# Kernel tuning notes

Hardware: AMD Instinct MI355X
Metric: run time of the kernel (lower is better)

## Reference

```python
import jax, jax.numpy as jnp
import numpy as np

N = 32767      # 2**15 - 1 nodes: complete binary tree, parent(i) = (i-1)//2
IN = 512       # in_channels
H = 256        # hidden_dim
OUT = 1        # output_dim
DEPTH = 15     # number of topological levels (static)


def setup_inputs() -> dict:
    key = jax.random.key(0)
    ks = jax.random.split(key, 8)
    x = jax.random.normal(ks[0], (N, IN), dtype=jnp.float32)
    # complete binary tree edge list: edge_index[0]=child, edge_index[1]=parent
    src = jnp.arange(1, N, dtype=jnp.int32)
    dst = (src - 1) // 2
    edge_index = jnp.stack([src, dst])  # [2, N-1]
    s = 1.0 / np.sqrt(H)  # torch LSTMCell/Linear default uniform init scale
    W_ih = jax.random.uniform(ks[1], (4 * H, IN), minval=-s, maxval=s, dtype=jnp.float32)
    W_hh = jax.random.uniform(ks[2], (4 * H, H), minval=-s, maxval=s, dtype=jnp.float32)
    b_ih = jax.random.uniform(ks[3], (4 * H,), minval=-s, maxval=s, dtype=jnp.float32)
    b_hh = jax.random.uniform(ks[4], (4 * H,), minval=-s, maxval=s, dtype=jnp.float32)
    W_fc = jax.random.uniform(ks[5], (OUT, H), minval=-s, maxval=s, dtype=jnp.float32)
    b_fc = jax.random.uniform(ks[6], (OUT,), minval=-s, maxval=s, dtype=jnp.float32)
    return {"x": x, "edge_index": edge_index, "W_ih": W_ih, "W_hh": W_hh,
            "b_ih": b_ih, "b_hh": b_hh, "W_fc": W_fc, "b_fc": b_fc}


def reference(x, edge_index, W_ih, W_hh, b_ih, b_hh, W_fc, b_fc):
    src, dst = edge_index[0], edge_index[1]
    # children count per parent (matches torch children_count loop)
    cnt = jax.ops.segment_sum(jnp.ones_like(src, dtype=x.dtype), dst, num_segments=N)
    cnt = jnp.maximum(cnt, 1.0)[:, None]  # [N,1]; leaves get zero child state anyway
    h = jnp.zeros((N, H), dtype=x.dtype)
    c = jnp.zeros((N, H), dtype=x.dtype)
    # topological sweep: deepest level first (children processed before parents)
    for d in range(DEPTH - 1, -1, -1):
        lo = 2 ** d - 1
        hi = min(2 ** (d + 1) - 1, N)  # level d node index range (static)
        # mean of already-computed child h/c states, gathered via edge list
        mean_h = jax.ops.segment_sum(h[src], dst, num_segments=N)[lo:hi] / cnt[lo:hi]
        mean_c = jax.ops.segment_sum(c[src], dst, num_segments=N)[lo:hi] / cnt[lo:hi]
        # torch LSTMCell: gates in (i, f, g, o) order
        gates = x[lo:hi] @ W_ih.T + b_ih + mean_h @ W_hh.T + b_hh  # [n_level, 4H]
        i, f, g, o = jnp.split(gates, 4, axis=-1)
        i, f, o = jax.nn.sigmoid(i), jax.nn.sigmoid(f), jax.nn.sigmoid(o)
        g = jnp.tanh(g)
        c_new = f * mean_c + i * g
        h_new = o * jnp.tanh(c_new)
        h = h.at[lo:hi].set(h_new)
        c = c.at[lo:hi].set(c_new)
    pooled = jnp.mean(h, axis=0, keepdims=True)  # [1, H]
    out = pooled @ W_fc.T + b_fc                 # [1, 1]
    return out.squeeze(-1)                       # [1]
```

## Files before the change

### kernel.cpp

```cpp
#include <hip/hip_runtime.h>
#include <hip/hip_cooperative_groups.h>
#include <math.h>

namespace cg = cooperative_groups;


#define N_NODES 32767
#define N_LEAF0 16383
#define IN_C    512
#define H_C     256

typedef __bf16 bf16x8 __attribute__((ext_vector_type(8)));
typedef __bf16 bf16x4 __attribute__((ext_vector_type(4)));
typedef float  f32x4  __attribute__((ext_vector_type(4)));

__device__ __forceinline__ void gload_lds16(const void* g, void* l) {
    __builtin_amdgcn_global_load_lds(
        (const __attribute__((address_space(1))) unsigned int*)g,
        (__attribute__((address_space(3))) unsigned int*)l,
        16, 0, 0);
}

__device__ __forceinline__ float fast_rcp(float x) { return __builtin_amdgcn_rcpf(x); }
__device__ __forceinline__ float sigm(float x)     { return fast_rcp(1.f + __expf(-x)); }
__device__ __forceinline__ float tanh_fast(float x){ return 2.f * fast_rcp(1.f + __expf(-2.f * x)) - 1.f; }

__global__ __launch_bounds__(256)
void conv2(const float* __restrict__ a, __bf16* __restrict__ da, int n8a,
           const float* __restrict__ b, __bf16* __restrict__ db, int n8b,
           float* __restrict__ hsum)
{
    if (blockIdx.x == 0 && threadIdx.x < 256) hsum[threadIdx.x] = 0.f;
    const int total = n8a + n8b;
    for (int i = blockIdx.x * 256 + threadIdx.x; i < total; i += gridDim.x * 256) {
        const float* s; __bf16* d; int j;
        if (i < n8a) { s = a; d = da; j = i; }
        else         { s = b; d = db; j = i - n8a; }
        const float4* s4 = (const float4*)s;
        const float4 v0 = s4[2 * j];
        const float4 v1 = s4[2 * j + 1];
        bf16x8 o;
        o[0] = (__bf16)v0.x; o[1] = (__bf16)v0.y; o[2] = (__bf16)v0.z; o[3] = (__bf16)v0.w;
        o[4] = (__bf16)v1.x; o[5] = (__bf16)v1.y; o[6] = (__bf16)v1.z; o[7] = (__bf16)v1.w;
        *(bf16x8*)(d + 8 * j) = o;
    }
}

__global__ __launch_bounds__(256)
void bulk_xw(const float* __restrict__ x,
             const __bf16* __restrict__ wih,
             const float* __restrict__ b_ih,
             const float* __restrict__ b_hh,
             __bf16* __restrict__ hb,
             float* __restrict__ c,
             __bf16* __restrict__ gx,
             float* __restrict__ hsum)
{
    __shared__ __bf16 As[128 * 64];
    __shared__ __bf16 Bs[128 * 64];
    __shared__ float  hs[32];

    const int t    = threadIdx.x;
    const int lane = t & 63;
    const int wv   = t >> 6;
    const int wm   = wv >> 1;
    const int wn   = wv & 1;
    const int quad = lane >> 4;
    const int l15  = lane & 15;

    if (t < 32) hs[t] = 0.f;

    const int i  = blockIdx.x;
    const int cb = (i >> 3) & 7;
    const int mt = (i & 7) | ((i >> 6) << 3);
    const int m0 = mt * 128;

    f32x4 acc[4][4];
#pragma unroll
    for (int mi = 0; mi < 4; ++mi)
#pragma unroll
        for (int ni = 0; ni < 4; ++ni) acc[mi][ni] = (f32x4)0.f;

    const int arow = t >> 1;
    const int kh   = (t & 1) * 32;
    const int anode = min(m0 + arow, N_NODES - 1);
    const float* xrow = x + (size_t)anode * IN_C + kh;
    float4 xr[8];
#pragma unroll
    for (int j = 0; j < 8; ++j) xr[j] = ((const float4*)xrow)[j];

    for (int k0 = 0; k0 < IN_C; k0 += 64) {
#pragma unroll
        for (int e = 0; e < 4; ++e) {
            const int ch = (wv * 4 + e) * 64 + lane;
            const int nl = ch >> 3;
            const int k8 = (ch & 7) ^ (nl & 7);
            const int q  = (nl >> 4) & 3;
            const int cc = (nl & 15) | ((nl >> 6) << 4);
            const int grow = q * H_C + cb * 32 + cc;
            gload_lds16(wih + (size_t)grow * IN_C + k0 + k8 * 8,
                        (char*)Bs + (wv * 4 + e) * 1024);
        }
#pragma unroll
        for (int j = 0; j < 4; ++j) {
            const float4 v0 = xr[2 * j], v1 = xr[2 * j + 1];
            bf16x8 o;
            o[0] = (__bf16)v0.x; o[1] = (__bf16)v0.y; o[2] = (__bf16)v0.z; o[3] = (__bf16)v0.w;
            o[4] = (__bf16)v1.x; o[5] = (__bf16)v1.y; o[6] = (__bf16)v1.z; o[7] = (__bf16)v1.w;
            const int cs = ((kh >> 3) + j) ^ (arow & 7);
            *(bf16x8*)(As + arow * 64 + cs * 8) = o;
        }
        __syncthreads();
        if (k0 + 64 < IN_C) {
            const float4* xs = (const float4*)(xrow + k0 + 64);
#pragma unroll
            for (int j = 0; j < 8; ++j) xr[j] = xs[j];
        }
#pragma unroll
        for (int ks = 0; ks < 2; ++ks) {
            bf16x8 af[4], bfr[4];
#pragma unroll
            for (int mi = 0; mi < 4; ++mi) {
                const int row = wm * 64 + mi * 16 + l15;
                af[mi] = *(const bf16x8*)(As + row * 64 + (((ks * 4 + quad) ^ (row & 7)) << 3));
            }
#pragma unroll
            for (int ni = 0; ni < 4; ++ni) {
                const int row = wn * 64 + ni * 16 + l15;
                bfr[ni] = *(const bf16x8*)(Bs + row * 64 + (((ks * 4 + quad) ^ (row & 7)) << 3));
            }
#pragma unroll
            for (int mi = 0; mi < 4; ++mi)
#pragma unroll
                for (int ni = 0; ni < 4; ++ni)
                    acc[mi][ni] = __builtin_amdgcn_mfma_f32_16x16x32_bf16(
                        af[mi], bfr[ni], acc[mi][ni], 0, 0, 0);
        }
        __syncthreads();
    }

    const int CH = cb * 32 + wn * 16 + l15;
    float bs4[4];
#pragma unroll
    for (int q = 0; q < 4; ++q) bs4[q] = b_ih[q * H_C + CH] + b_hh[q * H_C + CH];

    float lh = 0.f;
#pragma unroll
    for (int mi = 0; mi < 4; ++mi) {
#pragma unroll
        for (int r = 0; r < 4; ++r) {
            const int m = m0 + wm * 64 + mi * 16 + quad * 4 + r;
            if (m >= N_NODES) continue;
            if (m >= N_LEAF0) {
                const float gi = sigm(acc[mi][0][r] + bs4[0]);
                const float gg = tanh_fast(acc[mi][2][r] + bs4[2]);
                const float go = sigm(acc[mi][3][r] + bs4[3]);
                const float cn = gi * gg;
                const float hn = go * tanh_fast(cn);
                c[(size_t)m * H_C + CH] = cn;
                hb[(size_t)m * H_C + CH] = (__bf16)hn;
                lh += hn;
            } else {
                bf16x4 o;
#pragma unroll
                for (int q = 0; q < 4; ++q) o[q] = (__bf16)acc[mi][q][r];
                *(bf16x4*)(gx + ((size_t)m * H_C + CH) * 4) = o;
            }
        }
    }
    atomicAdd(&hs[wn * 16 + l15], lh);
    __syncthreads();
    if (t < 32) atomicAdd(&hsum[cb * 32 + t], hs[t]);
}

__device__ __forceinline__ void level_tile(
    const __bf16* __restrict__ whh, const float* __restrict__ b_ih,
    const float* __restrict__ b_hh, const __bf16* __restrict__ gx,
    __bf16* __restrict__ hb, float* __restrict__ c, float* __restrict__ hsum,
    __bf16* As, __bf16* Bs, float* hs, int lo, int n, int cb, int m0)
{
    const int t    = threadIdx.x;
    const int lane = t & 63;
    const int wv   = t >> 6;
    const int wm   = wv >> 1;
    const int wn   = wv & 1;
    const int quad = lane >> 4;
    const int l15  = lane & 15;

    f32x4 acc[4][4];
#pragma unroll
    for (int mi = 0; mi < 4; ++mi)
#pragma unroll
        for (int ni = 0; ni < 4; ++ni) acc[mi][ni] = (f32x4)0.f;

    for (int k0 = 0; k0 < H_C; k0 += 64) {
#pragma unroll
        for (int e = 0; e < 4; ++e) {
            const int ch = (wv * 4 + e) * 64 + lane;
            const int nl = ch >> 3;
            const int k8 = (ch & 7) ^ (nl & 7);
            const int q  = (nl >> 4) & 3;
            const int cc = (nl & 15) | ((nl >> 6) << 4);
            const int grow = q * H_C + cb * 32 + cc;
            gload_lds16(whh + (size_t)grow * H_C + k0 + k8 * 8,
                        (char*)Bs + (wv * 4 + e) * 1024);
        }
        {
            const int row  = t >> 1;
            const int kh   = (t & 1) * 32;
            const int node = lo + m0 + row;
            const int k2   = k0 + kh;
            const bf16x8* hl = (const bf16x8*)(hb + (size_t)(2 * node + 1) * H_C + k2);
            const bf16x8* hr = (const bf16x8*)(hb + (size_t)(2 * node + 2) * H_C + k2);
#pragma unroll
            for (int j = 0; j < 4; ++j) {
                const bf16x8 a = hl[j], b = hr[j];
                bf16x8 o;
#pragma unroll
                for (int e2 = 0; e2 < 8; ++e2)
                    o[e2] = (__bf16)(0.5f * ((float)a[e2] + (float)b[e2]));
                const int cs = ((kh >> 3) + j) ^ (row & 7);
                *(bf16x8*)(As + row * 64 + cs * 8) = o;
            }
        }
        __syncthreads();
#pragma unroll
        for (int ks = 0; ks < 2; ++ks) {
            bf16x8 af[4], bfr[4];
#pragma unroll
            for (int mi = 0; mi < 4; ++mi) {
                const int row = wm * 64 + mi * 16 + l15;
                af[mi] = *(const bf16x8*)(As + row * 64 + (((ks * 4 + quad) ^ (row & 7)) << 3));
            }
#pragma unroll
            for (int ni = 0; ni < 4; ++ni) {
                const int row = wn * 64 + ni * 16 + l15;
                bfr[ni] = *(const bf16x8*)(Bs + row * 64 + (((ks * 4 + quad) ^ (row & 7)) << 3));
            }
#pragma unroll
            for (int mi = 0; mi < 4; ++mi)
#pragma unroll
                for (int ni = 0; ni < 4; ++ni)
                    acc[mi][ni] = __builtin_amdgcn_mfma_f32_16x16x32_bf16(
                        af[mi], bfr[ni], acc[mi][ni], 0, 0, 0);
        }
        __syncthreads();
    }

    const int CH = cb * 32 + wn * 16 + l15;
    float bs4[4];
#pragma unroll
    for (int q = 0; q < 4; ++q) bs4[q] = b_ih[q * H_C + CH] + b_hh[q * H_C + CH];

    float lh = 0.f;
#pragma unroll
    for (int mi = 0; mi < 4; ++mi) {
#pragma unroll
        for (int r = 0; r < 4; ++r) {
            const int m = m0 + wm * 64 + mi * 16 + quad * 4 + r;
            if (m < n) {
                const int node = lo + m;
                const bf16x4 gv = *(const bf16x4*)(gx + ((size_t)node * H_C + CH) * 4);
                const float gi = sigm(acc[mi][0][r] + (float)gv[0] + bs4[0]);
                const float gf = sigm(acc[mi][1][r] + (float)gv[1] + bs4[1]);
                const float gg = tanh_fast(acc[mi][2][r] + (float)gv[2] + bs4[2]);
                const float go = sigm(acc[mi][3][r] + (float)gv[3] + bs4[3]);
                const float mc = 0.5f * (c[(size_t)(2 * node + 1) * H_C + CH] +
                                         c[(size_t)(2 * node + 2) * H_C + CH]);
                const float cn = gf * mc + gi * gg;
                const float hn = go * tanh_fast(cn);
                c[(size_t)node * H_C + CH] = cn;
                hb[(size_t)node * H_C + CH] = (__bf16)hn;
                lh += hn;
            }
        }
    }
    atomicAdd(&hs[wn * 16 + l15], lh);
    __syncthreads();
    if (t < 32) atomicAdd(&hsum[cb * 32 + t], hs[t]);
}

__global__ __launch_bounds__(256)
void level_hw(const __bf16* __restrict__ whh,
              const float* __restrict__ b_ih,
              const float* __restrict__ b_hh,
              const __bf16* __restrict__ gx,
              __bf16* __restrict__ hb,
              float* __restrict__ c,
              float* __restrict__ hsum,
              int lo, int n)
{
    __shared__ __bf16 As[128 * 64];
    __shared__ __bf16 Bs[128 * 64];
    __shared__ float  hs[32];
    if (threadIdx.x < 32) hs[threadIdx.x] = 0.f;
    const int i = blockIdx.x;
    int cb, mt;
    if (gridDim.x >= 64) { cb = (i >> 3) & 7; mt = (i & 7) | ((i >> 6) << 3); }
    else                 { cb = i & 7;        mt = i >> 3; }
    level_tile(whh, b_ih, b_hh, gx, hb, c, hsum, As, Bs, hs, lo, n, cb, mt * 128);
}

__global__ __launch_bounds__(256, 1)
void tail_levels(const __bf16* __restrict__ whh,
                 const float* __restrict__ b_ih,
                 const float* __restrict__ b_hh,
                 const __bf16* __restrict__ gx,
                 __bf16* __restrict__ hb,
                 float* __restrict__ c,
                 float* __restrict__ hsum,
                 const float* __restrict__ W_fc,
                 const float* __restrict__ b_fc,
                 float* __restrict__ out)
{
    __shared__ __bf16 Ws[128][264];
    __shared__ __align__(16) char UAG[64 * 264 * 2];
    __shared__ float cl[2][64][33];
    __shared__ float hs[32];
    __shared__ float fm[256];

    const int t    = threadIdx.x;
    const int cb   = blockIdx.x;
    const int lane = t & 63;
    const int wq   = t >> 6;
    const int quad = lane >> 4;
    const int l15  = lane & 15;

    auto As = (__bf16(*)[264])UAG;
    auto Gs = (float(*)[64][33])UAG;

    if (t < 32) hs[t] = 0.f;

    {
        const int row = t >> 1;
        const int k0  = (t & 1) * 128;
        const int q   = row >> 5, cc = row & 31;
        const __bf16* src = whh + (size_t)(q * H_C + cb * 32 + cc) * H_C + k0;
#pragma unroll
        for (int j = 0; j < 16; ++j)
            *(bf16x8*)(&Ws[row][k0 + 8 * j]) = *(const bf16x8*)(src + 8 * j);
    }
    const int ecc = t & 31;
    const int erg = t >> 5;
    const int CH  = cb * 32 + ecc;
    float bsq[4];
#pragma unroll
    for (int q = 0; q < 4; ++q) bsq[q] = b_ih[q * H_C + CH] + b_hh[q * H_C + CH];
    float th = 0.f;

    cg::grid_group grid = cg::this_grid();

    for (int d = 9; d >= 0; --d) {
        const int n   = 1 << d;
        const int lo  = n - 1;
        const int pp  = d & 1;
        const int nck = (n + 63) >> 6;
        for (int ck = 0; ck < nck; ++ck) {
            const int rbase = ck * 64;
            const int rows  = (n - rbase < 64) ? (n - rbase) : 64;
            __syncthreads();
            {
                const int row  = t >> 2;
                const int kb   = (t & 3) * 64;
                const int node = lo + rbase + row;
                const bf16x8* hl = (const bf16x8*)(hb + (size_t)(2 * node + 1) * H_C + kb);
                const bf16x8* hr = (const bf16x8*)(hb + (size_t)(2 * node + 2) * H_C + kb);
#pragma unroll
                for (int j = 0; j < 8; ++j) {
                    const bf16x8 a = hl[j], b = hr[j];
                    bf16x8 o;
#pragma unroll
                    for (int e = 0; e < 8; ++e)
                        o[e] = (__bf16)(0.5f * ((float)a[e] + (float)b[e]));
                    *(bf16x8*)(&As[row][kb + 8 * j]) = o;
                }
            }
            __syncthreads();
            f32x4 acc[4][2];
#pragma unroll
            for (int mi = 0; mi < 4; ++mi)
#pragma unroll
                for (int ni = 0; ni < 2; ++ni) acc[mi][ni] = (f32x4)0.f;
            for (int kk = 0; kk < 8; ++kk) {
#pragma unroll
                for (int mi = 0; mi < 4; ++mi) {
                    const bf16x8 af = *(const bf16x8*)(&As[mi * 16 + l15][kk * 32 + quad * 8]);
#pragma unroll
                    for (int ni = 0; ni < 2; ++ni) {
                        const bf16x8 bf_ = *(const bf16x8*)(&Ws[wq * 32 + ni * 16 + l15][kk * 32 + quad * 8]);
                        acc[mi][ni] = __builtin_amdgcn_mfma_f32_16x16x32_bf16(af, bf_, acc[mi][ni], 0, 0, 0);
                    }
                }
            }
            __syncthreads();
#pragma unroll
            for (int mi = 0; mi < 4; ++mi)
#pragma unroll
                for (int ni = 0; ni < 2; ++ni)
#pragma unroll
                    for (int r = 0; r < 4; ++r)
                        Gs[wq][mi * 16 + quad * 4 + r][ni * 16 + l15] = acc[mi][ni][r];
            __syncthreads();
            for (int r = erg; r < rows; r += 8) {
                const int rr   = rbase + r;
                const int node = lo + rr;
                const bf16x4 gv = *(const bf16x4*)(gx + ((size_t)node * H_C + CH) * 4);
                float g[4];
#pragma unroll
                for (int q = 0; q < 4; ++q) g[q] = Gs[q][r][ecc] + (float)gv[q] + bsq[q];
                const float gi = sigm(g[0]);
                const float gf = sigm(g[1]);
                const float gg = tanh_fast(g[2]);
                const float go = sigm(g[3]);
                float mc;
                if (d >= 6)
                    mc = 0.5f * (c[(size_t)(2 * node + 1) * H_C + CH] +
                                 c[(size_t)(2 * node + 2) * H_C + CH]);
                else
                    mc = 0.5f * (cl[pp ^ 1][2 * rr][ecc] + cl[pp ^ 1][2 * rr + 1][ecc]);
                const float cn = gf * mc + gi * gg;
                const float hn = go * tanh_fast(cn);
                if (d >= 7) c[(size_t)node * H_C + CH] = cn;
                else        cl[pp][rr][ecc] = cn;
                hb[(size_t)node * H_C + CH] = (__bf16)hn;
                th += hn;
            }
        }
        grid.sync();
    }

    atomicAdd(&hs[ecc], th);
    __syncthreads();
    if (t < 32) atomicAdd(&hsum[cb * 32 + t], hs[t]);
    grid.sync();

    if (cb == 0) {
        fm[t] = hsum[t] * (1.0f / (float)N_NODES) * W_fc[t];
        __syncthreads();
        for (int st = 128; st > 0; st >>= 1) {
            if (t < st) fm[t] += fm[t + st];
            __syncthreads();
        }
        if (t == 0) out[0] = fm[0] + b_fc[0];
    }
}

__global__ __launch_bounds__(256)
void final_out(const float* __restrict__ hsum,
               const float* __restrict__ W_fc,
               const float* __restrict__ b_fc,
               float* __restrict__ out)
{
    __shared__ float fm[256];
    const int t = threadIdx.x;
    fm[t] = hsum[t] * (1.0f / (float)N_NODES) * W_fc[t];
    __syncthreads();
    for (int st = 128; st > 0; st >>= 1) {
        if (t < st) fm[t] += fm[t + st];
        __syncthreads();
    }
    if (t == 0) out[0] = fm[0] + b_fc[0];
}

extern "C" void kernel_launch(void* const* d_in, const int* in_sizes, int n_in,
                              void* d_out, int out_size, void* d_ws, size_t ws_size,
                              hipStream_t stream)
{
    const float* x    = (const float*)d_in[0];
    const float* W_ih = (const float*)d_in[2];
    const float* W_hh = (const float*)d_in[3];
    const float* b_ih = (const float*)d_in[4];
    const float* b_hh = (const float*)d_in[5];
    const float* W_fc = (const float*)d_in[6];
    const float* b_fc = (const float*)d_in[7];
    float* out = (float*)d_out;

    char* w = (char*)d_ws;
    size_t used = 0;
    __bf16* hb   = (__bf16*)(w + used); used += (size_t)N_NODES * H_C * 2;
    float*  c    = (float*)(w + used);  used += (size_t)N_NODES * H_C * 4;
    __bf16* gx   = (__bf16*)(w + used); used += (size_t)N_LEAF0 * H_C * 4 * 2;
    __bf16* wihb = (__bf16*)(w + used); used += (size_t)4 * H_C * IN_C * 2;
    __bf16* whhb = (__bf16*)(w + used); used += (size_t)4 * H_C * H_C * 2;
    float*  hsum = (float*)(w + used);  used += 256 * 4;

    {
        const int n8i = (4 * H_C * IN_C) / 8;
        const int n8h = (4 * H_C * H_C) / 8;
        conv2<<<384, 256, 0, stream>>>(W_ih, wihb, n8i, W_hh, whhb, n8h, hsum);
    }

    bulk_xw<<<2048, 256, 0, stream>>>(x, wihb, b_ih, b_hh, hb, c, gx, hsum);

    for (int d = 13; d >= 10; --d) {
        const int n  = 1 << d;
        const int lo = n - 1;
        const int nm = (n + 127) / 128;
        level_hw<<<nm * 8, 256, 0, stream>>>(whhb, b_ih, b_hh, gx, hb, c, hsum, lo, n);
    }

    {
        const __bf16* a0 = whhb; const float* a1 = b_ih; const float* a2 = b_hh;
        const __bf16* a3 = gx;   __bf16* a4 = hb;        float* a5 = c;
        float* a6 = hsum;        const float* a7 = W_fc; const float* a8 = b_fc;
        float* a9 = out;
        void* targs[] = {&a0, &a1, &a2, &a3, &a4, &a5, &a6, &a7, &a8, &a9};
        hipError_t e = hipLaunchCooperativeKernel((const void*)tail_levels,
                                                  dim3(8), dim3(256), targs, 0, stream);
        if (e != hipSuccess) {
            for (int d = 9; d >= 0; --d) {
                const int n  = 1 << d;
                const int lo = n - 1;
                const int nm = (n + 127) / 128;
                level_hw<<<nm * 8, 256, 0, stream>>>(whhb, b_ih, b_hh, gx, hb, c, hsum, lo, n);
            }
            final_out<<<1, 256, 0, stream>>>(hsum, W_fc, b_fc, out);
        }
    }
}
```

Measured before the change: 465.3 us.

## Replace cooperative tail with single-block register-resident tail for top levels

The 8-block cooperative kernel that handled levels 9..0 with grid-wide syncs is replaced. Levels 9..7 now run as ordinary per-level launches, and a single 1024-thread block handles levels 6..0. That block keeps W_hh fragments in registers, keeps child h/c states in LDS, and folds the child mean into the MFMA by accumulating both children and scaling by 0.5. This removes grid.sync latency and global round trips for the small top levels, at the cost of three more launches and a serial single-CU tail. The bulk_xw x-tile load is also changed from register prefetch to a direct load inside each k-step.

Result: slower. 762.5 us (+63.9%).

```diff
diff --git a/kernel.cpp b/kernel.cpp
--- a/kernel.cpp
+++ b/kernel.cpp
@@ -1,8 +1,5 @@
 #include <hip/hip_runtime.h>
-#include <hip/hip_cooperative_groups.h>
 #include <math.h>
-
-namespace cg = cooperative_groups;
 
 
 #define N_NODES 32767
@@ -81,14 +78,6 @@
 #pragma unroll
         for (int ni = 0; ni < 4; ++ni) acc[mi][ni] = (f32x4)0.f;
 
-    const int arow = t >> 1;
-    const int kh   = (t & 1) * 32;
-    const int anode = min(m0 + arow, N_NODES - 1);
-    const float* xrow = x + (size_t)anode * IN_C + kh;
-    float4 xr[8];
-#pragma unroll
-    for (int j = 0; j < 8; ++j) xr[j] = ((const float4*)xrow)[j];
-
     for (int k0 = 0; k0 < IN_C; k0 += 64) {
 #pragma unroll
         for (int e = 0; e < 4; ++e) {
@@ -101,21 +90,22 @@
             gload_lds16(wih + (size_t)grow * IN_C + k0 + k8 * 8,
                         (char*)Bs + (wv * 4 + e) * 1024);
         }
-#pragma unroll
-        for (int j = 0; j < 4; ++j) {
-            const float4 v0 = xr[2 * j], v1 = xr[2 * j + 1];
-            bf16x8 o;
-            o[0] = (__bf16)v0.x; o[1] = (__bf16)v0.y; o[2] = (__bf16)v0.z; o[3] = (__bf16)v0.w;
-            o[4] = (__bf16)v1.x; o[5] = (__bf16)v1.y; o[6] = (__bf16)v1.z; o[7] = (__bf16)v1.w;
-            const int cs = ((kh >> 3) + j) ^ (arow & 7);
-            *(bf16x8*)(As + arow * 64 + cs * 8) = o;
-        }
-        __syncthreads();
-        if (k0 + 64 < IN_C) {
-            const float4* xs = (const float4*)(xrow + k0 + 64);
-#pragma unroll
-            for (int j = 0; j < 8; ++j) xr[j] = xs[j];
-        }
+        {
+            const int row  = t >> 1;
+            const int kh   = (t & 1) * 32;
+            const int node = min(m0 + row, N_NODES - 1);
+            const float4* xs = (const float4*)(x + (size_t)node * IN_C + k0 + kh);
+#pragma unroll
+            for (int j = 0; j < 4; ++j) {
+                const float4 v0 = xs[2 * j], v1 = xs[2 * j + 1];
+                bf16x8 o;
+                o[0] = (__bf16)v0.x; o[1] = (__bf16)v0.y; o[2] = (__bf16)v0.z; o[3] = (__bf16)v0.w;
+                o[4] = (__bf16)v1.x; o[5] = (__bf16)v1.y; o[6] = (__bf16)v1.z; o[7] = (__bf16)v1.w;
+                const int cs = ((kh >> 3) + j) ^ (row & 7);
+                *(bf16x8*)(As + row * 64 + cs * 8) = o;
+            }
+        }
+        __syncthreads();
 #pragma unroll
         for (int ks = 0; ks < 2; ++ks) {
             bf16x8 af[4], bfr[4];
@@ -301,165 +291,128 @@
     level_tile(whh, b_ih, b_hh, gx, hb, c, hsum, As, Bs, hs, lo, n, cb, mt * 128);
 }
 
-__global__ __launch_bounds__(256, 1)
-void tail_levels(const __bf16* __restrict__ whh,
-                 const float* __restrict__ b_ih,
-                 const float* __restrict__ b_hh,
-                 const __bf16* __restrict__ gx,
-                 __bf16* __restrict__ hb,
-                 float* __restrict__ c,
-                 float* __restrict__ hsum,
-                 const float* __restrict__ W_fc,
-                 const float* __restrict__ b_fc,
-                 float* __restrict__ out)
-{
-    __shared__ __bf16 Ws[128][264];
-    __shared__ __align__(16) char UAG[64 * 264 * 2];
-    __shared__ float cl[2][64][33];
-    __shared__ float hs[32];
-    __shared__ float fm[256];
+__global__ __launch_bounds__(1024)
+void tail1(const __bf16* __restrict__ whh,
+           const float* __restrict__ b_ih,
+           const float* __restrict__ b_hh,
+           const __bf16* __restrict__ gx,
+           const __bf16* __restrict__ hb,
+           const float* __restrict__ c,
+           const float* __restrict__ hsum,
+           const float* __restrict__ W_fc,
+           const float* __restrict__ b_fc,
+           float* __restrict__ out)
+{
+    __shared__ __bf16 Hout[64 * 256];
+    __shared__ float  Cc[64][260];
+    __shared__ float  fm[256];
+    __shared__ float  rm[256];
 
     const int t    = threadIdx.x;
-    const int cb   = blockIdx.x;
+    const int w    = t >> 6;
     const int lane = t & 63;
-    const int wq   = t >> 6;
     const int quad = lane >> 4;
     const int l15  = lane & 15;
-
-    auto As = (__bf16(*)[264])UAG;
-    auto Gs = (float(*)[64][33])UAG;
-
-    if (t < 32) hs[t] = 0.f;
-
-    {
-        const int row = t >> 1;
-        const int k0  = (t & 1) * 128;
-        const int q   = row >> 5, cc = row & 31;
-        const __bf16* src = whh + (size_t)(q * H_C + cb * 32 + cc) * H_C + k0;
-#pragma unroll
-        for (int j = 0; j < 16; ++j)
-            *(bf16x8*)(&Ws[row][k0 + 8 * j]) = *(const bf16x8*)(src + 8 * j);
-    }
-    const int ecc = t & 31;
-    const int erg = t >> 5;
-    const int CH  = cb * 32 + ecc;
+    const int ch   = w * 16 + l15;
+
+    if (t < 256) fm[t] = 0.f;
+
+    bf16x8 bq[4][8];
+#pragma unroll
+    for (int q = 0; q < 4; ++q)
+#pragma unroll
+        for (int kk = 0; kk < 8; ++kk)
+            bq[q][kk] = *(const bf16x8*)(whh + (size_t)(q * H_C + ch) * H_C + kk * 32 + quad * 8);
+
     float bsq[4];
 #pragma unroll
-    for (int q = 0; q < 4; ++q) bsq[q] = b_ih[q * H_C + CH] + b_hh[q * H_C + CH];
+    for (int q = 0; q < 4; ++q) bsq[q] = b_ih[q * H_C + ch] + b_hh[q * H_C + ch];
+
     float th = 0.f;
 
-    cg::grid_group grid = cg::this_grid();
-
-    for (int d = 9; d >= 0; --d) {
-        const int n   = 1 << d;
-        const int lo  = n - 1;
-        const int pp  = d & 1;
-        const int nck = (n + 63) >> 6;
-        for (int ck = 0; ck < nck; ++ck) {
-            const int rbase = ck * 64;
-            const int rows  = (n - rbase < 64) ? (n - rbase) : 64;
-            __syncthreads();
-            {
-                const int row  = t >> 2;
-                const int kb   = (t & 3) * 64;
-                const int node = lo + rbase + row;
-                const bf16x8* hl = (const bf16x8*)(hb + (size_t)(2 * node + 1) * H_C + kb);
-                const bf16x8* hr = (const bf16x8*)(hb + (size_t)(2 * node + 2) * H_C + kb);
-#pragma unroll
-                for (int j = 0; j < 8; ++j) {
-                    const bf16x8 a = hl[j], b = hr[j];
-                    bf16x8 o;
-#pragma unroll
-                    for (int e = 0; e < 8; ++e)
-                        o[e] = (__bf16)(0.5f * ((float)a[e] + (float)b[e]));
-                    *(bf16x8*)(&As[row][kb + 8 * j]) = o;
-                }
-            }
-            __syncthreads();
-            f32x4 acc[4][2];
-#pragma unroll
-            for (int mi = 0; mi < 4; ++mi)
-#pragma unroll
-                for (int ni = 0; ni < 2; ++ni) acc[mi][ni] = (f32x4)0.f;
-            for (int kk = 0; kk < 8; ++kk) {
-#pragma unroll
-                for (int mi = 0; mi < 4; ++mi) {
-                    const bf16x8 af = *(const bf16x8*)(&As[mi * 16 + l15][kk * 32 + quad * 8]);
-#pragma unroll
-                    for (int ni = 0; ni < 2; ++ni) {
-                        const bf16x8 bf_ = *(const bf16x8*)(&Ws[wq * 32 + ni * 16 + l15][kk * 32 + quad * 8]);
-                        acc[mi][ni] = __builtin_amdgcn_mfma_f32_16x16x32_bf16(af, bf_, acc[mi][ni], 0, 0, 0);
+    for (int d = 6; d >= 0; --d) {
+        const int n      = 1 << d;
+        const int lo     = n - 1;
+        const int mtiles = (n + 15) >> 4;
+
+        f32x4 acc[4][4];
+#pragma unroll
+        for (int mi = 0; mi < 4; ++mi)
+#pragma unroll
+            for (int q = 0; q < 4; ++q) acc[mi][q] = (f32x4)0.f;
+
+#pragma unroll
+        for (int mi = 0; mi < 4; ++mi) {
+            if (mi < mtiles) {
+                const int R = mi * 16 + l15;
+#pragma unroll
+                for (int kk = 0; kk < 8; ++kk) {
+                    bf16x8 a0, a1;
+                    if (d == 6) {
+                        a0 = *(const bf16x8*)(hb + (size_t)(127 + 2 * R) * H_C + kk * 32 + quad * 8);
+                        a1 = *(const bf16x8*)(hb + (size_t)(128 + 2 * R) * H_C + kk * 32 + quad * 8);
+                    } else {
+                        const int ck = kk * 4 + quad;
+                        a0 = *(const bf16x8*)(Hout + (2 * R) * 256 + ((ck ^ ((2 * R) & 31)) & 31) * 8);
+                        a1 = *(const bf16x8*)(Hout + (2 * R + 1) * 256 + ((ck ^ ((2 * R + 1) & 31)) & 31) * 8);
+                    }
+#pragma unroll
+                    for (int q = 0; q < 4; ++q) {
+                        acc[mi][q] = __builtin_amdgcn_mfma_f32_16x16x32_bf16(a0, bq[q][kk], acc[mi][q], 0, 0, 0);
+                        acc[mi][q] = __builtin_amdgcn_mfma_f32_16x16x32_bf16(a1, bq[q][kk], acc[mi][q], 0, 0, 0);
                     }
                 }
             }
-            __syncthreads();
-#pragma unroll
-            for (int mi = 0; mi < 4; ++mi)
-#pragma unroll
-                for (int ni = 0; ni < 2; ++ni)
-#pragma unroll
-                    for (int r = 0; r < 4; ++r)
-                        Gs[wq][mi * 16 + quad * 4 + r][ni * 16 + l15] = acc[mi][ni][r];
-            __syncthreads();
-            for (int r = erg; r < rows; r += 8) {
-                const int rr   = rbase + r;
-                const int node = lo + rr;
-                const bf16x4 gv = *(const bf16x4*)(gx + ((size_t)node * H_C + CH) * 4);
-                float g[4];
-#pragma unroll
-                for (int q = 0; q < 4; ++q) g[q] = Gs[q][r][ecc] + (float)gv[q] + bsq[q];
-                const float gi = sigm(g[0]);
-                const float gf = sigm(g[1]);
-                const float gg = tanh_fast(g[2]);
-                const float go = sigm(g[3]);
-                float mc;
-                if (d >= 6)
-                    mc = 0.5f * (c[(size_t)(2 * node + 1) * H_C + CH] +
-                                 c[(size_t)(2 * node + 2) * H_C + CH]);
-                else
-                    mc = 0.5f * (cl[pp ^ 1][2 * rr][ecc] + cl[pp ^ 1][2 * rr + 1][ecc]);
-                const float cn = gf * mc + gi * gg;
-                const float hn = go * tanh_fast(cn);
-                if (d >= 7) c[(size_t)node * H_C + CH] = cn;
-                else        cl[pp][rr][ecc] = cn;
-                hb[(size_t)node * H_C + CH] = (__bf16)hn;
-                th += hn;
-            }
-        }
-        grid.sync();
-    }
-
-    atomicAdd(&hs[ecc], th);
+        }
+        float mc[4][4];
+#pragma unroll
+        for (int mi = 0; mi < 4; ++mi) {
+#pragma unroll
+            for (int r = 0; r < 4; ++r) {
+                const int row = mi * 16 + quad * 4 + r;
+                if (mi < mtiles) {
+                    if (d == 6)
+                        mc[mi][r] = 0.5f * (c[(size_t)(127 + 2 * row) * H_C + ch] +
+                                            c[(size_t)(128 + 2 * row) * H_C + ch]);
+                    else
+                        mc[mi][r] = 0.5f * (Cc[2 * row][ch] + Cc[2 * row + 1][ch]);
+                } else mc[mi][r] = 0.f;
+            }
+        }
+        __syncthreads();
+#pragma unroll
+        for (int mi = 0; mi < 4; ++mi) {
+#pragma unroll
+            for (int r = 0; r < 4; ++r) {
+                const int row = mi * 16 + quad * 4 + r;
+                if (mi < mtiles && row < n) {
+                    const int node = lo + row;
+                    const bf16x4 gv = *(const bf16x4*)(gx + ((size_t)node * H_C + ch) * 4);
+                    const float gi = sigm(0.5f * acc[mi][0][r] + (float)gv[0] + bsq[0]);
+                    const float gf = sigm(0.5f * acc[mi][1][r] + (float)gv[1] + bsq[1]);
+                    const float gg = tanh_fast(0.5f * acc[mi][2][r] + (float)gv[2] + bsq[2]);
+                    const float go = sigm(0.5f * acc[mi][3][r] + (float)gv[3] + bsq[3]);
+                    const float cn = gf * mc[mi][r] + gi * gg;
+                    const float hn = go * tanh_fast(cn);
+                    Cc[row][ch] = cn;
+                    const int ck = ch >> 3;
+                    Hout[row * 256 + ((ck ^ (row & 31)) & 31) * 8 + (ch & 7)] = (__bf16)hn;
+                    th += hn;
+                }
+            }
+        }
+        __syncthreads();
+    }
+
+    atomicAdd(&fm[ch], th);
     __syncthreads();
-    if (t < 32) atomicAdd(&hsum[cb * 32 + t], hs[t]);
-    grid.sync();
-
-    if (cb == 0) {
-        fm[t] = hsum[t] * (1.0f / (float)N_NODES) * W_fc[t];
-        __syncthreads();
-        for (int st = 128; st > 0; st >>= 1) {
-            if (t < st) fm[t] += fm[t + st];
-            __syncthreads();
-        }
-        if (t == 0) out[0] = fm[0] + b_fc[0];
-    }
-}
-
-__global__ __launch_bounds__(256)
-void final_out(const float* __restrict__ hsum,
-               const float* __restrict__ W_fc,
-               const float* __restrict__ b_fc,
-               float* __restrict__ out)
-{
-    __shared__ float fm[256];
-    const int t = threadIdx.x;
-    fm[t] = hsum[t] * (1.0f / (float)N_NODES) * W_fc[t];
+    if (t < 256) rm[t] = (fm[t] + hsum[t]) * (1.0f / (float)N_NODES) * W_fc[t];
     __syncthreads();
     for (int st = 128; st > 0; st >>= 1) {
-        if (t < st) fm[t] += fm[t + st];
-        __syncthreads();
-    }
-    if (t == 0) out[0] = fm[0] + b_fc[0];
+        if (t < st) rm[t] += rm[t + st];
+        __syncthreads();
+    }
+    if (t == 0) out[0] = rm[0] + b_fc[0];
 }
 
 extern "C" void kernel_launch(void* const* d_in, const int* in_sizes, int n_in,
@@ -492,29 +445,12 @@
 
     bulk_xw<<<2048, 256, 0, stream>>>(x, wihb, b_ih, b_hh, hb, c, gx, hsum);
 
-    for (int d = 13; d >= 10; --d) {
+    for (int d = 13; d >= 7; --d) {
         const int n  = 1 << d;
         const int lo = n - 1;
         const int nm = (n + 127) / 128;
         level_hw<<<nm * 8, 256, 0, stream>>>(whhb, b_ih, b_hh, gx, hb, c, hsum, lo, n);
     }
 
-    {
-        const __bf16* a0 = whhb; const float* a1 = b_ih; const float* a2 = b_hh;
-        const __bf16* a3 = gx;   __bf16* a4 = hb;        float* a5 = c;
-        float* a6 = hsum;        const float* a7 = W_fc; const float* a8 = b_fc;
-        float* a9 = out;
-        void* targs[] = {&a0, &a1, &a2, &a3, &a4, &a5, &a6, &a7, &a8, &a9};
-        hipError_t e = hipLaunchCooperativeKernel((const void*)tail_levels,
-                                                  dim3(8), dim3(256), targs, 0, stream);
-        if (e != hipSuccess) {
-            for (int d = 9; d >= 0; --d) {
-                const int n  = 1 << d;
-                const int lo = n - 1;
-                const int nm = (n + 127) / 128;
-                level_hw<<<nm * 8, 256, 0, stream>>>(whhb, b_ih, b_hh, gx, hb, c, hsum, lo, n);
-            }
-            final_out<<<1, 256, 0, stream>>>(hsum, W_fc, b_fc, out);
-        }
-    }
-}
+    tail1<<<1, 1024, 0, stream>>>(whhb, b_ih, b_hh, gx, hb, c, hsum, W_fc, b_fc, out);
+}
```
